# Performance work log

Hardware: AMD Instinct MI355X
Metric: run time of the kernel (lower is better)

The kernel has to match this reference:

```python
import jax, jax.numpy as jnp
import numpy as np

D_MODEL = 1024
NUM_HEADS = 16
D_K = 64
D_FF = 4096
EPS = 1e-6  # source says eps=1-6 (typo); 1e-6 intended
NEG_INF = 1.0e9


def layer_norm(x, g, b):
    mu = jnp.mean(x, axis=-1, keepdims=True)
    var = jnp.mean(jnp.square(x - mu), axis=-1, keepdims=True)
    return (x - mu) * jax.lax.rsqrt(var + EPS) * g + b


def setup_inputs() -> dict:
    key = jax.random.key(0)
    ks = jax.random.split(key, 12)
    B, L, D, F = 8, 1024, D_MODEL, D_FF
    s = 0.02
    return {
        "x": jax.random.normal(ks[0], (B, L, D), jnp.float32),
        "e_mask": jnp.ones((B, 1, L), jnp.int32),
        "ln1_g": jnp.ones((D,), jnp.float32),
        "ln1_b": jnp.zeros((D,), jnp.float32),
        "Wq": jax.random.normal(ks[1], (D, D), jnp.float32) * s,
        "bq": jnp.zeros((D,), jnp.float32),
        "Wk": jax.random.normal(ks[2], (D, D), jnp.float32) * s,
        "bk": jnp.zeros((D,), jnp.float32),
        "Wv": jax.random.normal(ks[3], (D, D), jnp.float32) * s,
        "bv": jnp.zeros((D,), jnp.float32),
        "Wo": jax.random.normal(ks[4], (D, D), jnp.float32) * s,
        "bo": jnp.zeros((D,), jnp.float32),
        "ln2_g": jnp.ones((D,), jnp.float32),
        "ln2_b": jnp.zeros((D,), jnp.float32),
        "W1": jax.random.normal(ks[5], (D, F), jnp.float32) * s,
        "b1": jnp.zeros((F,), jnp.float32),
        "W2": jax.random.normal(ks[6], (F, D), jnp.float32) * s,
        "b2": jnp.zeros((D,), jnp.float32),
    }


def reference(x, e_mask, ln1_g, ln1_b, Wq, bq, Wk, bk, Wv, bv, Wo, bo,
              ln2_g, ln2_b, W1, b1, W2, b2):
    B, L, D = x.shape
    H, Dk = NUM_HEADS, D_K

    # pre-LN self-attention
    x1 = layer_norm(x, ln1_g, ln1_b)
    q = (x1 @ Wq + bq).reshape(B, L, H, Dk).transpose(0, 2, 1, 3)  # [B,H,L,Dk]
    k = (x1 @ Wk + bk).reshape(B, L, H, Dk).transpose(0, 2, 1, 3)
    v = (x1 @ Wv + bv).reshape(B, L, H, Dk).transpose(0, 2, 1, 3)

    scores = jnp.einsum("bhqd,bhkd->bhqk", q, k) / jnp.sqrt(jnp.float32(Dk))
    mask = e_mask[:, None, :, :]  # [B,1,1,L] broadcasts over heads & queries
    scores = jnp.where(mask == 0, -NEG_INF, scores)
    probs = jax.nn.softmax(scores, axis=-1)  # dropout = identity (eval)
    attn = jnp.einsum("bhqk,bhkd->bhqd", probs, v)
    attn = attn.transpose(0, 2, 1, 3).reshape(B, L, D)
    x = x + (attn @ Wo + bo)

    # pre-LN FFN
    x2 = layer_norm(x, ln2_g, ln2_b)
    h = jax.nn.relu(x2 @ W1 + b1)
    x = x + (h @ W2 + b2)
    return x
```

## Files before the change

### kernel.cpp

```cpp
#include <hip/hip_runtime.h>
#include <hip/hip_bf16.h>

typedef __attribute__((ext_vector_type(4))) float f32x4;
typedef __attribute__((ext_vector_type(8))) short short8;
typedef __attribute__((ext_vector_type(4))) short short4v;
typedef __attribute__((ext_vector_type(2))) unsigned int u32x2;
typedef unsigned short ushort_t;

__device__ __forceinline__ f32x4 mfma16(short8 a, short8 b, f32x4 c) {
  return __builtin_amdgcn_mfma_f32_16x16x32_bf16(a, b, c, 0, 0, 0);
}

__device__ __forceinline__ void gload_lds16(const void* g, void* l) {
  __builtin_amdgcn_global_load_lds(
      (const __attribute__((address_space(1))) void*)g,
      (__attribute__((address_space(3))) void*)l, 16, 0, 0);
}

__device__ __forceinline__ ushort_t f2bf(float f) {
  union { float f; unsigned int u; } un; un.f = f;
  unsigned int u = un.u;
  u += 0x7fffu + ((u >> 16) & 1u);
  return (ushort_t)(u >> 16);
}

__device__ __forceinline__ float fast_exp2(float x) {
#if __has_builtin(__builtin_amdgcn_exp2f)
  return __builtin_amdgcn_exp2f(x);
#else
  return exp2f(x);
#endif
}

__device__ __forceinline__ unsigned int cvt_pk_bf16(float a, float b) {
  unsigned int r;
  asm("v_cvt_pk_bf16_f32 %0, %1, %2" : "=v"(r) : "v"(a), "v"(b));
  return r;
}

__global__ __launch_bounds__(256) void tcvt_ker(const float* __restrict__ in,
                                                ushort_t* __restrict__ out,
                                                int R, int C) {
  __shared__ float t[64][65];
  const int tid = threadIdx.x;
  const int tr = blockIdx.y * 64;
  const int tc = blockIdx.x * 64;
#pragma unroll
  for (int it = 0; it < 4; ++it) {
    int r = it * 16 + (tid >> 4);
    int c4 = (tid & 15) * 4;
    f32x4 v = *(const f32x4*)&in[(size_t)(tr + r) * C + tc + c4];
#pragma unroll
    for (int e = 0; e < 4; ++e) t[r][c4 + e] = v[e];
  }
  __syncthreads();
#pragma unroll
  for (int it = 0; it < 4; ++it) {
    int idx = it * 256 + tid;
    int n = idx >> 4;
    int k4 = (idx & 15) * 4;
    short4v o;
#pragma unroll
    for (int e = 0; e < 4; ++e) o[e] = (short)f2bf(t[k4 + e][n]);
    *(short4v*)&out[(size_t)(tc + n) * R + tr + k4] = o;
  }
}

__global__ __launch_bounds__(256) void concat3_ker(const float* __restrict__ a,
                                                   const float* __restrict__ b,
                                                   const float* __restrict__ c,
                                                   float* __restrict__ o) {
  int i = blockIdx.x * 256 + threadIdx.x;
  if (i < 3072) o[i] = i < 1024 ? a[i] : (i < 2048 ? b[i - 1024] : c[i - 2048]);
}

__global__ __launch_bounds__(256) void mbias_ker(const int* __restrict__ emask,
                                                 float* __restrict__ mb) {
  int i = blockIdx.x * 256 + threadIdx.x;
  if (i < 8192) mb[i] = emask[i] ? 0.f : -1e9f;
}

__global__ __launch_bounds__(256) void ln_ker(const float* __restrict__ x,
                                              const float* __restrict__ g,
                                              const float* __restrict__ b,
                                              ushort_t* __restrict__ out) {
  const int wave = threadIdx.x >> 6, lane = threadIdx.x & 63;
  const size_t row = (size_t)blockIdx.x * 4 + wave;
  const float* xr = x + row * 1024;
  f32x4 v[4];
  float s = 0.f, sq = 0.f;
#pragma unroll
  for (int jj = 0; jj < 4; ++jj) {
    v[jj] = *(const f32x4*)&xr[lane * 4 + jj * 256];
#pragma unroll
    for (int e = 0; e < 4; ++e) { s += v[jj][e]; sq += v[jj][e] * v[jj][e]; }
  }
#pragma unroll
  for (int off = 1; off < 64; off <<= 1) {
    s += __shfl_xor(s, off);
    sq += __shfl_xor(sq, off);
  }
  const float mu = s * (1.0f / 1024.0f);
  const float var = sq * (1.0f / 1024.0f) - mu * mu;
  const float rst = rsqrtf(var + 1e-6f);
#pragma unroll
  for (int jj = 0; jj < 4; ++jj) {
    int col = lane * 4 + jj * 256;
    f32x4 gv = *(const f32x4*)&g[col];
    f32x4 bv = *(const f32x4*)&b[col];
    short4v o;
#pragma unroll
    for (int e = 0; e < 4; ++e)
      o[e] = (short)f2bf((v[jj][e] - mu) * rst * gv[e] + bv[e]);
    *(short4v*)&out[row * 1024 + col] = o;
  }
}

__global__ __launch_bounds__(256) void vtrans_ker(const ushort_t* __restrict__ qkv,
                                                  ushort_t* __restrict__ vt) {
  __shared__ ushort_t l[64][72];
  const int tid = threadIdx.x;
  const int tile = blockIdx.x;
  const int bh = blockIdx.y;
  const int b = bh >> 4, h = bh & 15;
  const size_t base = (size_t)b * 1024 * 3072 + 2048 + h * 64;
#pragma unroll
  for (int it = 0; it < 2; ++it) {
    int idx = it * 256 + tid;
    int row = idx >> 3, c8 = (idx & 7) * 8;
    short8 v = *(const short8*)(qkv + base + (size_t)(tile * 64 + row) * 3072 + c8);
    *(short8*)&l[row][c8] = v;
  }
  __syncthreads();
#pragma unroll
  for (int it = 0; it < 2; ++it) {
    int idx = it * 256 + tid;
    int d = idx >> 3, k0 = (idx & 7) * 8;
    short8 o;
#pragma unroll
    for (int m = 0; m < 8; ++m) {
      int kp = k0 + m;
      int key = (kp & 3) * 16 + (kp >> 2);
      o[m] = (short)l[key][d];
    }
    *(short8*)&vt[((size_t)bh * 64 + d) * 1024 + tile * 64 + k0] = o;
  }
}

template <int MODE, int BM, int BN>
__global__ __launch_bounds__(512, 1) void gemm8_ker(
    const ushort_t* __restrict__ A, const ushort_t* __restrict__ Bt,
    const float* __restrict__ bias, const float* __restrict__ resid,
    void* __restrict__ Cout, int M, int N, int K) {
  constexpr int MR = BM / 32;
  constexpr int NR = BN / 64;
  constexpr int LA = BM / 128;
  constexpr int LB = BN / 128;
  constexpr int HALF_A = (BM / 2) * 128;
  constexpr int HALF_B = (BN / 2) * 128;
  constexpr int TILE = 2 * HALF_A + 2 * HALF_B;
  constexpr int VN = LA + 2 * LB;

  __shared__ alignas(128) char lds[2 * TILE];

  const int tid = threadIdx.x;
  const int wave = tid >> 6, lane = tid & 63;
  const int g = lane >> 4, l15 = lane & 15;
  const int wr = wave >> 2, wc = wave & 3;

  const int nwg = gridDim.x * gridDim.y;
  int wg = blockIdx.y * gridDim.x + blockIdx.x;
  if ((nwg & 7) == 0) wg = (wg & 7) * (nwg >> 3) + (wg >> 3);
  const int bx = wg % gridDim.x, by = wg / gridDim.x;
  const int mbase = by * BM;
  const int nbase = bx * BN;
  const int NT = K >> 6;

  auto stage_A = [&](int bf, int h, int kt) {
    const ushort_t* sb = A + (size_t)(mbase + h * (BM / 2)) * K + kt * 64;
    char* dst = lds + bf * TILE + h * HALF_A;
#pragma unroll
    for (int it = 0; it < LA; ++it) {
      int li = it * 512 + tid;
      int r = li >> 3;
      int cs = ((tid & 7) * 16) ^ ((r & 7) << 4);
      gload_lds16((const char*)(sb + (size_t)r * K) + cs, dst + li * 16);
    }
  };
  auto stage_B = [&](int bf, int h, int kt) {
    const ushort_t* sb = Bt + (size_t)(nbase + h * (BN / 2)) * K + kt * 64;
    char* dst = lds + bf * TILE + 2 * HALF_A + h * HALF_B;
#pragma unroll
    for (int it = 0; it < LB; ++it) {
      int li = it * 512 + tid;
      int r = li >> 3;
      int cs = ((tid & 7) * 16) ^ ((r & 7) << 4);
      gload_lds16((const char*)(sb + (size_t)r * K) + cs, dst + li * 16);
    }
  };
  auto frag = [&](const char* slot, int r, int kk) -> short8 {
    const int cb = kk * 64 + g * 16;
    return *(const short8*)(slot + r * 128 + (cb ^ ((r & 7) << 4)));
  };

  f32x4 acc[MR][NR];
  const f32x4 zf = {0.f, 0.f, 0.f, 0.f};
#pragma unroll
  for (int i = 0; i < MR; ++i)
#pragma unroll
    for (int j = 0; j < NR; ++j) acc[i][j] = zf;

  stage_A(0, 0, 0); stage_A(0, 1, 0); stage_B(0, 0, 0); stage_B(0, 1, 0);
  stage_A(1, 0, 1); stage_B(1, 0, 1); stage_B(1, 1, 1);
  asm volatile("s_waitcnt vmcnt(%0)" :: "n"(VN) : "memory");
  __builtin_amdgcn_s_barrier();

  short8 fa[MR / 2][2], fb0[NR / 2][2], fb1[NR / 2][2];

  for (int t = 0; t < NT; ++t) {
    const int buf = t & 1;
    const int k1 = (t + 1 < NT) ? t + 1 : NT - 1;
    const int k2 = (t + 2 < NT) ? t + 2 : NT - 1;
    const char* sA0 = lds + buf * TILE;
    const char* sA1 = sA0 + HALF_A;
    const char* sB0 = sA0 + 2 * HALF_A;
    const char* sB1 = sB0 + HALF_B;

#pragma unroll
    for (int ii = 0; ii < MR / 2; ++ii)
#pragma unroll
      for (int kk = 0; kk < 2; ++kk)
        fa[ii][kk] = frag(sA0, wr * (BM / 4) + ii * 16 + l15, kk);
#pragma unroll
    for (int jj = 0; jj < NR / 2; ++jj)
#pragma unroll
      for (int kk = 0; kk < 2; ++kk)
        fb0[jj][kk] = frag(sB0, wc * (BN / 8) + jj * 16 + l15, kk);
    stage_A(buf ^ 1, 1, k1);
    __builtin_amdgcn_s_barrier();
    __builtin_amdgcn_sched_barrier(0);
    __builtin_amdgcn_s_setprio(1);
#pragma unroll
    for (int ii = 0; ii < MR / 2; ++ii)
#pragma unroll
      for (int jj = 0; jj < NR / 2; ++jj)
#pragma unroll
        for (int kk = 0; kk < 2; ++kk)
          acc[ii][jj] = mfma16(fa[ii][kk], fb0[jj][kk], acc[ii][jj]);
    __builtin_amdgcn_s_setprio(0);
    __builtin_amdgcn_sched_barrier(0);
#pragma unroll
    for (int jj = 0; jj < NR / 2; ++jj)
#pragma unroll
      for (int kk = 0; kk < 2; ++kk)
        fb1[jj][kk] = frag(sB1, wc * (BN / 8) + jj * 16 + l15, kk);
    __builtin_amdgcn_sched_barrier(0);
    __builtin_amdgcn_s_barrier();

    stage_A(buf, 0, k2);
    __builtin_amdgcn_s_barrier();
    __builtin_amdgcn_sched_barrier(0);
    __builtin_amdgcn_s_setprio(1);
#pragma unroll
    for (int ii = 0; ii < MR / 2; ++ii)
#pragma unroll
      for (int jj = 0; jj < NR / 2; ++jj)
#pragma unroll
        for (int kk = 0; kk < 2; ++kk)
          acc[ii][jj + NR / 2] = mfma16(fa[ii][kk], fb1[jj][kk], acc[ii][jj + NR / 2]);
    __builtin_amdgcn_s_setprio(0);
    __builtin_amdgcn_sched_barrier(0);
#pragma unroll
    for (int ii = 0; ii < MR / 2; ++ii)
#pragma unroll
      for (int kk = 0; kk < 2; ++kk)
        fa[ii][kk] = frag(sA1, wr * (BM / 4) + ii * 16 + l15, kk);
    __builtin_amdgcn_sched_barrier(0);
    __builtin_amdgcn_s_barrier();

    stage_B(buf, 0, k2);
    stage_B(buf, 1, k2);
    __builtin_amdgcn_s_barrier();
    __builtin_amdgcn_sched_barrier(0);
    __builtin_amdgcn_s_setprio(1);
#pragma unroll
    for (int ii = 0; ii < MR / 2; ++ii)
#pragma unroll
      for (int jj = 0; jj < NR / 2; ++jj)
#pragma unroll
        for (int kk = 0; kk < 2; ++kk)
          acc[ii + MR / 2][jj + NR / 2] =
              mfma16(fa[ii][kk], fb1[jj][kk], acc[ii + MR / 2][jj + NR / 2]);
#pragma unroll
    for (int ii = 0; ii < MR / 2; ++ii)
#pragma unroll
      for (int jj = 0; jj < NR / 2; ++jj)
#pragma unroll
        for (int kk = 0; kk < 2; ++kk)
          acc[ii + MR / 2][jj] = mfma16(fa[ii][kk], fb0[jj][kk], acc[ii + MR / 2][jj]);
    __builtin_amdgcn_s_setprio(0);
    __builtin_amdgcn_sched_barrier(0);
    asm volatile("s_waitcnt vmcnt(%0)" :: "n"(VN) : "memory");
    __builtin_amdgcn_s_barrier();
  }

  asm volatile("s_waitcnt vmcnt(0)" ::: "memory");

  float bcol[NR];
#pragma unroll
  for (int j = 0; j < NR; ++j) {
    const int bandj = j / (NR / 2), jj = j % (NR / 2);
    bcol[j] = bias[nbase + bandj * (BN / 2) + wc * (BN / 8) + jj * 16 + l15];
  }
#pragma unroll
  for (int i = 0; i < MR; ++i) {
    const int band = i / (MR / 2), ii = i % (MR / 2);
    const int rowb = mbase + band * (BM / 2) + wr * (BM / 4) + ii * 16 + g * 4;
#pragma unroll
    for (int r = 0; r < 4; ++r) {
      const int row = rowb + r;
#pragma unroll
      for (int j = 0; j < NR; ++j) {
        const int bandj = j / (NR / 2), jj = j % (NR / 2);
        const int col = nbase + bandj * (BN / 2) + wc * (BN / 8) + jj * 16 + l15;
        float v = acc[i][j][r] + bcol[j];
        if (MODE == 2) {
          ((float*)Cout)[(size_t)row * N + col] = resid[(size_t)row * N + col] + v;
        } else {
          if (MODE == 1) v = fmaxf(v, 0.f);
          ((ushort_t*)Cout)[(size_t)row * N + col] = f2bf(v);
        }
      }
    }
  }
}

__global__ __launch_bounds__(256) void attn_ker(const ushort_t* __restrict__ qkv,
                                                const ushort_t* __restrict__ vt,
                                                const float* __restrict__ mbias,
                                                ushort_t* __restrict__ out) {
  __shared__ ushort_t lK[2][4096];
  __shared__ ushort_t lV[2][4096];
  __shared__ ushort_t lP[4][1024];
  const int tid = threadIdx.x;
  const int wave = tid >> 6, lane = tid & 63;
  const int g = lane >> 4, l15 = lane & 15;
  const int orig = blockIdx.y * 16 + blockIdx.x;
  const int swz = (orig & 7) * 256 + (orig >> 3);
  const int qt = swz & 15;
  const int bh = swz >> 4;
  const int b = bh >> 4, h = bh & 15;
  const int QS = 3072;
  const size_t base = (size_t)b * 1024 * QS;
  const int qoff = h * 64, koff = 1024 + h * 64;

  short8 qf[2];
  {
    const int qrow = qt * 64 + wave * 16 + l15;
    const ushort_t* qp = qkv + base + (size_t)qrow * QS + qoff + g * 8;
    qf[0] = *(const short8*)(qp);
    qf[1] = *(const short8*)(qp + 32);
  }
  f32x4 lsum4 = {0.f, 0.f, 0.f, 0.f};
  f32x4 acco[4];
  const f32x4 zf = {0.f, 0.f, 0.f, 0.f};
#pragma unroll
  for (int dj = 0; dj < 4; ++dj) acco[dj] = zf;

  const float SCL = 0.125f * 1.44269504089f;
  const float* mbp = mbias + b * 1024 + l15;

  const int itrow = tid >> 3;
  const int c16 = ((tid & 7) * 16) ^ ((itrow & 7) << 4);
  const char* srcK = (const char*)(qkv + base + (size_t)itrow * QS + koff) + c16;
  const char* srcV = (const char*)(vt + ((size_t)bh * 64 + itrow) * 1024) + c16;
  constexpr int K_IT = 32 * 3072 * 2;
  constexpr int K_T  = 64 * 3072 * 2;
  constexpr int V_IT = 32 * 1024 * 2;
  constexpr int V_T  = 64 * 2;

  auto stage = [&](int bufi) {
    gload_lds16(srcK, &lK[bufi][tid * 8]);
    gload_lds16(srcK + K_IT, &lK[bufi][2048 + tid * 8]);
    gload_lds16(srcV, &lV[bufi][tid * 8]);
    gload_lds16(srcV + V_IT, &lV[bufi][2048 + tid * 8]);
  };

  stage(0);
  srcK += K_T; srcV += V_T;
  __syncthreads();

  for (int t = 0; t < 16; ++t) {
    const int buf = t & 1;
    if (t < 15) {
      stage(buf ^ 1);
      srcK += K_T; srcV += V_T;
    }
    const int kv = t * 64;

    f32x4 s[4];
#pragma unroll
    for (int j = 0; j < 4; ++j) {
      const int row = j * 16 + l15;
      const int sw = (l15 & 7) << 3;
      const short8 b0 = *(const short8*)&lK[buf][row * 64 + ((g * 8) ^ sw)];
      const short8 b1 = *(const short8*)&lK[buf][row * 64 + ((32 + g * 8) ^ sw)];
      f32x4 t2 = mfma16(qf[0], b0, zf);
      t2 = mfma16(qf[1], b1, t2);
      const float bias = mbp[kv + j * 16];
#pragma unroll
      for (int e = 0; e < 4; ++e) t2[e] = t2[e] * SCL + bias;
      s[j] = t2;
    }

#pragma unroll
    for (int j = 0; j < 4; ++j) {
#pragma unroll
      for (int e = 0; e < 4; ++e) s[j][e] = fast_exp2(s[j][e]);
      lsum4 += s[j];
    }

    ushort_t* lPw = lP[wave];
#pragma unroll
    for (int r = 0; r < 4; ++r) {
      const int q = g * 4 + r;
      u32x2 pk;
      pk[0] = cvt_pk_bf16(s[0][r], s[1][r]);
      pk[1] = cvt_pk_bf16(s[2][r], s[3][r]);
      *(u32x2*)&lPw[q * 64 + ((l15 * 4) ^ ((q & 7) << 3))] = pk;
    }

#pragma unroll
    for (int kk = 0; kk < 2; ++kk) {
      const short8 pa =
          *(const short8*)&lPw[l15 * 64 + ((kk * 32 + g * 8) ^ ((l15 & 7) << 3))];
#pragma unroll
      for (int dj = 0; dj < 4; ++dj) {
        const int drow = dj * 16 + l15;
        const short8 vb =
            *(const short8*)&lV[buf][drow * 64 + ((kk * 32 + g * 8) ^ ((drow & 7) << 3))];
        acco[dj] = mfma16(pa, vb, acco[dj]);
      }
    }
    __syncthreads();
  }

#pragma unroll
  for (int r = 0; r < 4; ++r) {
    float tot = lsum4[r];
    tot += __shfl_xor(tot, 1);
    tot += __shfl_xor(tot, 2);
    tot += __shfl_xor(tot, 4);
    tot += __shfl_xor(tot, 8);
    const float inv = 1.0f / tot;
    const int row = qt * 64 + wave * 16 + g * 4 + r;
#pragma unroll
    for (int dj = 0; dj < 4; ++dj)
      out[((size_t)(b * 1024 + row)) * 1024 + h * 64 + dj * 16 + l15] =
          f2bf(acco[dj][r] * inv);
  }
}

extern "C" void kernel_launch(void* const* d_in, const int* in_sizes, int n_in,
                              void* d_out, int out_size, void* d_ws, size_t ws_size,
                              hipStream_t stream) {
  const float* x    = (const float*)d_in[0];
  const int* emask  = (const int*)d_in[1];
  const float* ln1g = (const float*)d_in[2];
  const float* ln1b = (const float*)d_in[3];
  const float* Wq   = (const float*)d_in[4];
  const float* bq   = (const float*)d_in[5];
  const float* Wk   = (const float*)d_in[6];
  const float* bk   = (const float*)d_in[7];
  const float* Wv   = (const float*)d_in[8];
  const float* bv   = (const float*)d_in[9];
  const float* Wo   = (const float*)d_in[10];
  const float* bo   = (const float*)d_in[11];
  const float* ln2g = (const float*)d_in[12];
  const float* ln2b = (const float*)d_in[13];
  const float* W1   = (const float*)d_in[14];
  const float* b1   = (const float*)d_in[15];
  const float* W2   = (const float*)d_in[16];
  const float* b2   = (const float*)d_in[17];

  char* p = (char*)d_ws;
  auto carve = [&](size_t bytes) {
    char* r = p;
    p += (bytes + 255) & ~(size_t)255;
    return r;
  };
  ushort_t* WqkvT = (ushort_t*)carve((size_t)3072 * 1024 * 2);
  ushort_t* WoT   = (ushort_t*)carve((size_t)1024 * 1024 * 2);
  ushort_t* W1T   = (ushort_t*)carve((size_t)4096 * 1024 * 2);
  ushort_t* W2T   = (ushort_t*)carve((size_t)1024 * 4096 * 2);
  float*    bqkv  = (float*)carve(3072 * 4);
  float*    mb    = (float*)carve(8192 * 4);
  ushort_t* x1    = (ushort_t*)carve((size_t)8192 * 1024 * 2);
  ushort_t* qkvb  = (ushort_t*)carve((size_t)8192 * 3072 * 2);
  ushort_t* attnb = (ushort_t*)carve((size_t)8192 * 1024 * 2);
  float*    xres  = (float*)carve((size_t)8192 * 1024 * 4);
  ushort_t* x2    = (ushort_t*)carve((size_t)8192 * 1024 * 2);
  ushort_t* hbuf  = (ushort_t*)carve((size_t)8192 * 4096 * 2);
  ushort_t* vtg   = x1;

  tcvt_ker<<<dim3(16, 16), 256, 0, stream>>>(Wq, WqkvT, 1024, 1024);
  tcvt_ker<<<dim3(16, 16), 256, 0, stream>>>(Wk, WqkvT + (size_t)1024 * 1024, 1024, 1024);
  tcvt_ker<<<dim3(16, 16), 256, 0, stream>>>(Wv, WqkvT + (size_t)2048 * 1024, 1024, 1024);
  tcvt_ker<<<dim3(16, 16), 256, 0, stream>>>(Wo, WoT, 1024, 1024);
  tcvt_ker<<<dim3(64, 16), 256, 0, stream>>>(W1, W1T, 1024, 4096);
  tcvt_ker<<<dim3(16, 64), 256, 0, stream>>>(W2, W2T, 4096, 1024);
  concat3_ker<<<12, 256, 0, stream>>>(bq, bk, bv, bqkv);
  mbias_ker<<<32, 256, 0, stream>>>(emask, mb);

  ln_ker<<<2048, 256, 0, stream>>>(x, ln1g, ln1b, x1);
  gemm8_ker<0, 256, 128><<<dim3(24, 32), 512, 0, stream>>>(x1, WqkvT, bqkv, nullptr,
                                                           qkvb, 8192, 3072, 1024);
  vtrans_ker<<<dim3(16, 128), 256, 0, stream>>>(qkvb, vtg);
  attn_ker<<<dim3(16, 128), 256, 0, stream>>>(qkvb, vtg, mb, attnb);
  gemm8_ker<2, 128, 128><<<dim3(8, 64), 512, 0, stream>>>(attnb, WoT, bo, x, xres,
                                                          8192, 1024, 1024);
  ln_ker<<<2048, 256, 0, stream>>>(xres, ln2g, ln2b, x2);
  gemm8_ker<1, 256, 256><<<dim3(16, 32), 512, 0, stream>>>(x2, W1T, b1, nullptr, hbuf,
                                                           8192, 4096, 1024);
  gemm8_ker<2, 128, 128><<<dim3(8, 64), 512, 0, stream>>>(hbuf, W2T, b2, xres,
                                                          (float*)d_out, 8192, 1024, 4096);
}
```

Before: 353.0 us.

## Process two query tiles per attention block and store residual in bf16

The attention kernel now handles 128 query rows per block (two 64-row sub-tiles) so each staged K/V tile is reused twice, halving K/V global loads and launching half as many blocks, with a launch-bounds occupancy hint. Separately, the intermediate residual after the output projection is stored as bf16 instead of fp32, with a new bf16 layernorm kernel and new GEMM epilogue modes. This cuts residual memory traffic but loses precision in the residual stream.

New measurement: 340.3 us. -3.6%, faster.

```diff
diff --git a/kernel.cpp b/kernel.cpp
--- a/kernel.cpp
+++ b/kernel.cpp
@@ -22,6 +22,11 @@
   unsigned int u = un.u;
   u += 0x7fffu + ((u >> 16) & 1u);
   return (ushort_t)(u >> 16);
+}
+
+__device__ __forceinline__ float bf2f(ushort_t u) {
+  union { unsigned int i; float f; } c; c.i = ((unsigned int)u) << 16;
+  return c.f;
 }
 
 __device__ __forceinline__ float fast_exp2(float x) {
@@ -116,6 +121,50 @@
   }
 }
 
+__global__ __launch_bounds__(256) void ln_bf16_ker(const ushort_t* __restrict__ x,
+                                                   const float* __restrict__ g,
+                                                   const float* __restrict__ b,
+                                                   ushort_t* __restrict__ out) {
+  const int wave = threadIdx.x >> 6, lane = threadIdx.x & 63;
+  const size_t row = (size_t)blockIdx.x * 4 + wave;
+  const ushort_t* xr = x + row * 1024;
+  float vf[16];
+  float s = 0.f, sq = 0.f;
+#pragma unroll
+  for (int jj = 0; jj < 2; ++jj) {
+    short8 v8 = *(const short8*)&xr[lane * 8 + jj * 512];
+#pragma unroll
+    for (int e = 0; e < 8; ++e) {
+      float f = bf2f((ushort_t)v8[e]);
+      vf[jj * 8 + e] = f;
+      s += f; sq += f * f;
+    }
+  }
+#pragma unroll
+  for (int off = 1; off < 64; off <<= 1) {
+    s += __shfl_xor(s, off);
+    sq += __shfl_xor(sq, off);
+  }
+  const float mu = s * (1.0f / 1024.0f);
+  const float var = sq * (1.0f / 1024.0f) - mu * mu;
+  const float rst = rsqrtf(var + 1e-6f);
+#pragma unroll
+  for (int jj = 0; jj < 2; ++jj) {
+    int col = lane * 8 + jj * 512;
+    short8 o;
+#pragma unroll
+    for (int q = 0; q < 2; ++q) {
+      f32x4 gv = *(const f32x4*)&g[col + q * 4];
+      f32x4 bv = *(const f32x4*)&b[col + q * 4];
+#pragma unroll
+      for (int e = 0; e < 4; ++e)
+        o[q * 4 + e] =
+            (short)f2bf((vf[jj * 8 + q * 4 + e] - mu) * rst * gv[e] + bv[e]);
+    }
+    *(short8*)&out[row * 1024 + col] = o;
+  }
+}
+
 __global__ __launch_bounds__(256) void vtrans_ker(const ushort_t* __restrict__ qkv,
                                                   ushort_t* __restrict__ vt) {
   __shared__ ushort_t l[64][72];
@@ -150,7 +199,7 @@
 template <int MODE, int BM, int BN>
 __global__ __launch_bounds__(512, 1) void gemm8_ker(
     const ushort_t* __restrict__ A, const ushort_t* __restrict__ Bt,
-    const float* __restrict__ bias, const float* __restrict__ resid,
+    const float* __restrict__ bias, const void* __restrict__ resid,
     void* __restrict__ Cout, int M, int N, int K) {
   constexpr int MR = BM / 32;
   constexpr int NR = BN / 64;
@@ -324,8 +373,12 @@
         const int bandj = j / (NR / 2), jj = j % (NR / 2);
         const int col = nbase + bandj * (BN / 2) + wc * (BN / 8) + jj * 16 + l15;
         float v = acc[i][j][r] + bcol[j];
-        if (MODE == 2) {
-          ((float*)Cout)[(size_t)row * N + col] = resid[(size_t)row * N + col] + v;
+        if (MODE == 4) {
+          float rv = bf2f(((const ushort_t*)resid)[(size_t)row * N + col]);
+          ((float*)Cout)[(size_t)row * N + col] = rv + v;
+        } else if (MODE == 3) {
+          float rv = ((const float*)resid)[(size_t)row * N + col];
+          ((ushort_t*)Cout)[(size_t)row * N + col] = f2bf(rv + v);
         } else {
           if (MODE == 1) v = fmaxf(v, 0.f);
           ((ushort_t*)Cout)[(size_t)row * N + col] = f2bf(v);
@@ -335,37 +388,42 @@
   }
 }
 
-__global__ __launch_bounds__(256) void attn_ker(const ushort_t* __restrict__ qkv,
-                                                const ushort_t* __restrict__ vt,
-                                                const float* __restrict__ mbias,
-                                                ushort_t* __restrict__ out) {
+__global__ __launch_bounds__(256, 4) void attn_ker(const ushort_t* __restrict__ qkv,
+                                                   const ushort_t* __restrict__ vt,
+                                                   const float* __restrict__ mbias,
+                                                   ushort_t* __restrict__ out) {
   __shared__ ushort_t lK[2][4096];
   __shared__ ushort_t lV[2][4096];
   __shared__ ushort_t lP[4][1024];
   const int tid = threadIdx.x;
   const int wave = tid >> 6, lane = tid & 63;
   const int g = lane >> 4, l15 = lane & 15;
-  const int orig = blockIdx.y * 16 + blockIdx.x;
-  const int swz = (orig & 7) * 256 + (orig >> 3);
-  const int qt = swz & 15;
-  const int bh = swz >> 4;
+  const int orig = blockIdx.y * 8 + blockIdx.x;
+  const int swz = (orig & 7) * 128 + (orig >> 3);
+  const int qp = swz & 7;
+  const int bh = swz >> 3;
   const int b = bh >> 4, h = bh & 15;
   const int QS = 3072;
   const size_t base = (size_t)b * 1024 * QS;
   const int qoff = h * 64, koff = 1024 + h * 64;
 
-  short8 qf[2];
-  {
-    const int qrow = qt * 64 + wave * 16 + l15;
-    const ushort_t* qp = qkv + base + (size_t)qrow * QS + qoff + g * 8;
-    qf[0] = *(const short8*)(qp);
-    qf[1] = *(const short8*)(qp + 32);
-  }
-  f32x4 lsum4 = {0.f, 0.f, 0.f, 0.f};
-  f32x4 acco[4];
+  short8 qf[2][2];
+#pragma unroll
+  for (int s = 0; s < 2; ++s) {
+    const int qrow = qp * 128 + s * 64 + wave * 16 + l15;
+    const ushort_t* qpt = qkv + base + (size_t)qrow * QS + qoff + g * 8;
+    qf[s][0] = *(const short8*)(qpt);
+    qf[s][1] = *(const short8*)(qpt + 32);
+  }
+  f32x4 lsum4[2];
+  f32x4 acco[2][4];
   const f32x4 zf = {0.f, 0.f, 0.f, 0.f};
 #pragma unroll
-  for (int dj = 0; dj < 4; ++dj) acco[dj] = zf;
+  for (int s = 0; s < 2; ++s) {
+    lsum4[s] = zf;
+#pragma unroll
+    for (int dj = 0; dj < 4; ++dj) acco[s][dj] = zf;
+  }
 
   const float SCL = 0.125f * 1.44269504089f;
   const float* mbp = mbias + b * 1024 + l15;
@@ -397,67 +455,75 @@
       srcK += K_T; srcV += V_T;
     }
     const int kv = t * 64;
-
-    f32x4 s[4];
-#pragma unroll
-    for (int j = 0; j < 4; ++j) {
-      const int row = j * 16 + l15;
-      const int sw = (l15 & 7) << 3;
-      const short8 b0 = *(const short8*)&lK[buf][row * 64 + ((g * 8) ^ sw)];
-      const short8 b1 = *(const short8*)&lK[buf][row * 64 + ((32 + g * 8) ^ sw)];
-      f32x4 t2 = mfma16(qf[0], b0, zf);
-      t2 = mfma16(qf[1], b1, t2);
-      const float bias = mbp[kv + j * 16];
-#pragma unroll
-      for (int e = 0; e < 4; ++e) t2[e] = t2[e] * SCL + bias;
-      s[j] = t2;
-    }
-
-#pragma unroll
-    for (int j = 0; j < 4; ++j) {
-#pragma unroll
-      for (int e = 0; e < 4; ++e) s[j][e] = fast_exp2(s[j][e]);
-      lsum4 += s[j];
-    }
+    float mbv[4];
+#pragma unroll
+    for (int j = 0; j < 4; ++j) mbv[j] = mbp[kv + j * 16];
 
     ushort_t* lPw = lP[wave];
 #pragma unroll
+    for (int s = 0; s < 2; ++s) {
+      f32x4 sv[4];
+#pragma unroll
+      for (int j = 0; j < 4; ++j) {
+        const int row = j * 16 + l15;
+        const int sw = (l15 & 7) << 3;
+        const short8 b0 = *(const short8*)&lK[buf][row * 64 + ((g * 8) ^ sw)];
+        const short8 b1 = *(const short8*)&lK[buf][row * 64 + ((32 + g * 8) ^ sw)];
+        f32x4 t2 = mfma16(qf[s][0], b0, zf);
+        t2 = mfma16(qf[s][1], b1, t2);
+#pragma unroll
+        for (int e = 0; e < 4; ++e) t2[e] = t2[e] * SCL + mbv[j];
+        sv[j] = t2;
+      }
+
+#pragma unroll
+      for (int j = 0; j < 4; ++j) {
+#pragma unroll
+        for (int e = 0; e < 4; ++e) sv[j][e] = fast_exp2(sv[j][e]);
+        lsum4[s] += sv[j];
+      }
+
+#pragma unroll
+      for (int r = 0; r < 4; ++r) {
+        const int q = g * 4 + r;
+        u32x2 pk;
+        pk[0] = cvt_pk_bf16(sv[0][r], sv[1][r]);
+        pk[1] = cvt_pk_bf16(sv[2][r], sv[3][r]);
+        *(u32x2*)&lPw[q * 64 + ((l15 * 4) ^ ((q & 7) << 3))] = pk;
+      }
+
+#pragma unroll
+      for (int kk = 0; kk < 2; ++kk) {
+        const short8 pa =
+            *(const short8*)&lPw[l15 * 64 + ((kk * 32 + g * 8) ^ ((l15 & 7) << 3))];
+#pragma unroll
+        for (int dj = 0; dj < 4; ++dj) {
+          const int drow = dj * 16 + l15;
+          const short8 vb =
+              *(const short8*)&lV[buf][drow * 64 + ((kk * 32 + g * 8) ^ ((drow & 7) << 3))];
+          acco[s][dj] = mfma16(pa, vb, acco[s][dj]);
+        }
+      }
+    }
+    __syncthreads();
+  }
+
+#pragma unroll
+  for (int s = 0; s < 2; ++s) {
+#pragma unroll
     for (int r = 0; r < 4; ++r) {
-      const int q = g * 4 + r;
-      u32x2 pk;
-      pk[0] = cvt_pk_bf16(s[0][r], s[1][r]);
-      pk[1] = cvt_pk_bf16(s[2][r], s[3][r]);
-      *(u32x2*)&lPw[q * 64 + ((l15 * 4) ^ ((q & 7) << 3))] = pk;
-    }
-
-#pragma unroll
-    for (int kk = 0; kk < 2; ++kk) {
-      const short8 pa =
-          *(const short8*)&lPw[l15 * 64 + ((kk * 32 + g * 8) ^ ((l15 & 7) << 3))];
-#pragma unroll
-      for (int dj = 0; dj < 4; ++dj) {
-        const int drow = dj * 16 + l15;
-        const short8 vb =
-            *(const short8*)&lV[buf][drow * 64 + ((kk * 32 + g * 8) ^ ((drow & 7) << 3))];
-        acco[dj] = mfma16(pa, vb, acco[dj]);
-      }
-    }
-    __syncthreads();
-  }
-
-#pragma unroll
-  for (int r = 0; r < 4; ++r) {
-    float tot = lsum4[r];
-    tot += __shfl_xor(tot, 1);
-    tot += __shfl_xor(tot, 2);
-    tot += __shfl_xor(tot, 4);
-    tot += __shfl_xor(tot, 8);
-    const float inv = 1.0f / tot;
-    const int row = qt * 64 + wave * 16 + g * 4 + r;
-#pragma unroll
-    for (int dj = 0; dj < 4; ++dj)
-      out[((size_t)(b * 1024 + row)) * 1024 + h * 64 + dj * 16 + l15] =
-          f2bf(acco[dj][r] * inv);
+      float tot = lsum4[s][r];
+      tot += __shfl_xor(tot, 1);
+      tot += __shfl_xor(tot, 2);
+      tot += __shfl_xor(tot, 4);
+      tot += __shfl_xor(tot, 8);
+      const float inv = 1.0f / tot;
+      const int row = qp * 128 + s * 64 + wave * 16 + g * 4 + r;
+#pragma unroll
+      for (int dj = 0; dj < 4; ++dj)
+        out[((size_t)(b * 1024 + row)) * 1024 + h * 64 + dj * 16 + l15] =
+            f2bf(acco[s][dj][r] * inv);
+    }
   }
 }
 
@@ -498,7 +564,7 @@
   ushort_t* x1    = (ushort_t*)carve((size_t)8192 * 1024 * 2);
   ushort_t* qkvb  = (ushort_t*)carve((size_t)8192 * 3072 * 2);
   ushort_t* attnb = (ushort_t*)carve((size_t)8192 * 1024 * 2);
-  float*    xres  = (float*)carve((size_t)8192 * 1024 * 4);
+  ushort_t* xres  = (ushort_t*)carve((size_t)8192 * 1024 * 2);
   ushort_t* x2    = (ushort_t*)carve((size_t)8192 * 1024 * 2);
   ushort_t* hbuf  = (ushort_t*)carve((size_t)8192 * 4096 * 2);
   ushort_t* vtg   = x1;
@@ -516,12 +582,12 @@
   gemm8_ker<0, 256, 128><<<dim3(24, 32), 512, 0, stream>>>(x1, WqkvT, bqkv, nullptr,
                                                            qkvb, 8192, 3072, 1024);
   vtrans_ker<<<dim3(16, 128), 256, 0, stream>>>(qkvb, vtg);
-  attn_ker<<<dim3(16, 128), 256, 0, stream>>>(qkvb, vtg, mb, attnb);
-  gemm8_ker<2, 128, 128><<<dim3(8, 64), 512, 0, stream>>>(attnb, WoT, bo, x, xres,
+  attn_ker<<<dim3(8, 128), 256, 0, stream>>>(qkvb, vtg, mb, attnb);
+  gemm8_ker<3, 128, 128><<<dim3(8, 64), 512, 0, stream>>>(attnb, WoT, bo, x, xres,
                                                           8192, 1024, 1024);
-  ln_ker<<<2048, 256, 0, stream>>>(xres, ln2g, ln2b, x2);
+  ln_bf16_ker<<<2048, 256, 0, stream>>>(xres, ln2g, ln2b, x2);
   gemm8_ker<1, 256, 256><<<dim3(16, 32), 512, 0, stream>>>(x2, W1T, b1, nullptr, hbuf,
                                                            8192, 4096, 1024);
-  gemm8_ker<2, 128, 128><<<dim3(8, 64), 512, 0, stream>>>(hbuf, W2T, b2, xres,
+  gemm8_ker<4, 128, 128><<<dim3(8, 64), 512, 0, stream>>>(hbuf, W2T, b2, xres,
                                                           (float*)d_out, 8192, 1024, 4096);
 }
```
